# Kernel optimization log

Hardware: AMD Instinct MI355X
Metric: run time of the kernel (lower is better)

Reference implementation:

```python
import jax, jax.numpy as jnp
import numpy as np

B, MAX_H, MAX_W, D, S, HID = 64, 64, 32, 512, 8, 64


def setup_inputs() -> dict:
    key = jax.random.key(0)
    ks = jax.random.split(key, 7)
    return {
        "canonical": jax.random.normal(ks[0], (S, S, D), jnp.float32) * 0.02,
        "w1": jax.random.normal(ks[1], (2, HID), jnp.float32) * 0.5,
        "b1": jax.random.normal(ks[2], (HID,), jnp.float32) * 0.1,
        "w2": jax.random.normal(ks[3], (HID, D), jnp.float32) * 0.05,
        "b2": jax.random.normal(ks[4], (D,), jnp.float32) * 0.05,
        "batch_size": B,
        "target_h_list": jax.random.randint(ks[5], (B,), 1, MAX_H + 1, jnp.int32),
        "target_w_list": jax.random.randint(ks[6], (B,), 1, MAX_W + 1, jnp.int32),
        "max_h": MAX_H,
        "max_w": MAX_W,
    }


def _axis_coords(sizes, max_len):
    # sizes: [B] clamped lengths; returns normalized coords u in [0,1] at each
    # padded position (torch.linspace(0,1,L) semantics; 0 when L==1). [B, max_len]
    idx = jnp.arange(max_len, dtype=jnp.float32)[None, :]
    L = sizes[:, None].astype(jnp.float32)
    return jnp.where(L > 1, idx / jnp.maximum(L - 1.0, 1.0), 0.0)


def _forward(canonical, w1, b1, w2, b2, target_h_list, target_w_list, max_h, max_w):
    S_ = canonical.shape[0]
    Hs = jnp.clip(target_h_list, 1, max_h)  # [B]
    Ws = jnp.clip(target_w_list, 1, max_w)  # [B]

    u = _axis_coords(Hs, max_h)  # [B, mh]
    v = _axis_coords(Ws, max_w)  # [B, mw]

    # Bilinear resize of canonical grid with align_corners=True:
    # source coord = normalized coord * (S-1)
    sy = jnp.clip(u * (S_ - 1), 0.0, S_ - 1.0)  # [B, mh]
    sx = jnp.clip(v * (S_ - 1), 0.0, S_ - 1.0)  # [B, mw]
    y0 = jnp.floor(sy).astype(jnp.int32)
    x0 = jnp.floor(sx).astype(jnp.int32)
    y1 = jnp.minimum(y0 + 1, S_ - 1)
    x1 = jnp.minimum(x0 + 1, S_ - 1)
    wy = (sy - y0.astype(jnp.float32))[:, :, None, None]  # [B, mh, 1, 1]
    wx = (sx - x0.astype(jnp.float32))[:, None, :, None]  # [B, 1, mw, 1]

    yi0 = y0[:, :, None]  # [B, mh, 1]
    yi1 = y1[:, :, None]
    xi0 = x0[:, None, :]  # [B, 1, mw]
    xi1 = x1[:, None, :]
    q00 = canonical[yi0, xi0]  # [B, mh, mw, D]
    q01 = canonical[yi0, xi1]
    q10 = canonical[yi1, xi0]
    q11 = canonical[yi1, xi1]
    bil = ((1.0 - wy) * ((1.0 - wx) * q00 + wx * q01)
           + wy * ((1.0 - wx) * q10 + wx * q11))  # [B, mh, mw, D]

    # Coordinate refinement MLP on (u, v)
    coords = jnp.stack(
        [jnp.broadcast_to(u[:, :, None], (u.shape[0], max_h, max_w)),
         jnp.broadcast_to(v[:, None, :], (u.shape[0], max_h, max_w))],
        axis=-1)  # [B, mh, mw, 2]
    h = jax.nn.gelu(coords @ w1 + b1, approximate=False)
    delta = h @ w2 + b2  # [B, mh, mw, D]

    mask = ((jnp.arange(max_h)[None, :, None] < Hs[:, None, None])
            & (jnp.arange(max_w)[None, None, :] < Ws[:, None, None]))  # [B, mh, mw]
    queries = jnp.where(mask[..., None], bil + delta, 0.0)
    return queries, mask


def reference(canonical, w1, b1, w2, b2, batch_size, target_h_list,
              target_w_list, max_h, max_w):
    return _forward(canonical, w1, b1, w2, b2, target_h_list, target_w_list,
                    max_h, max_w)
```

## Files before the change

kernel.cpp:

```cpp
#include <hip/hip_runtime.h>
#include <math.h>

#define NB    64
#define MAXH  64
#define MAXW  32
#define DCH   512
#define SS    8
#define HID   64

#define QTOTAL ((size_t)NB * MAXH * MAXW * DCH)

typedef float f4 __attribute__((ext_vector_type(4)));

__device__ __forceinline__ float gelu_exact(float x) {
    return 0.5f * x * (1.0f + erff(x * 0.70710678118654752440f));
}

__global__ __launch_bounds__(256) void hgqg_kernel(
    const float* __restrict__ canonical,
    const float* __restrict__ w1,
    const float* __restrict__ b1,
    const float* __restrict__ w2,
    const float* __restrict__ b2,
    const int*   __restrict__ hlist,
    const int*   __restrict__ wlist,
    float* __restrict__ out)
{
    const int blk = blockIdx.x;
    const int b   = blk >> 6;
    const int i   = blk & 63;
    const int t   = threadIdx.x;

    int H = hlist[b]; H = min(max(H, 1), MAXH);
    int W = wlist[b]; W = min(max(W, 1), MAXW);

    f4* q4 = (f4*)(out + (size_t)blk * (MAXW * DCH));

    if (t < MAXW) {
        out[QTOTAL + (size_t)blk * MAXW + t] = (i < H && t < W) ? 1.0f : 0.0f;
    }

    if (i >= H) {
        const f4 z = {0.f, 0.f, 0.f, 0.f};
        #pragma unroll
        for (int r = 0; r < 16; ++r)
            __builtin_nontemporal_store(z, q4 + t + r * 256);
        return;
    }

    const float u    = (H > 1) ? (float)i / (float)(H - 1) : 0.0f;
    const float sy   = fminf(u * 7.0f, 7.0f);
    const int   y0   = (int)sy;
    const int   y1   = min(y0 + 1, SS - 1);
    const float wy   = sy - (float)y0;
    const float winv = (W > 1) ? 1.0f / (float)(W - 1) : 0.0f;

    __shared__ f4 ri[SS * 128];
    {
        const f4* can4 = (const f4*)canonical;
        #pragma unroll
        for (int r = 0; r < 4; ++r) {
            const int idx = t + r * 256;
            const int x   = idx >> 7;
            const int c   = idx & 127;
            const f4 a = can4[(y0 * SS + x) * 128 + c];
            const f4 d = can4[(y1 * SS + x) * 128 + c];
            ri[idx] = a + wy * (d - a);
        }
    }

    __shared__ __align__(16) float hsh[MAXW][HID];
    {
        const int j  = t >> 3;
        const int k0 = (t & 7) * 8;
        const float v = (float)j * winv;
        #pragma unroll
        for (int kk = 0; kk < 8; ++kk) {
            const int k = k0 + kk;
            hsh[j][k] = gelu_exact(u * w1[k] + v * w1[HID + k] + b1[k]);
        }
    }
    __syncthreads();

    const int cid = t & 127;
    const int jg  = t >> 7;
    const f4  bb2 = ((const f4*)b2)[cid];

    f4 acc[16];

    #pragma unroll
    for (int s = 0; s < 16; ++s) {
        const int   j  = jg + 2 * s;
        const float v  = (float)j * winv;
        const float sx = fminf(v * 7.0f, 7.0f);
        const int   x0 = (int)sx;
        const int   x1 = min(x0 + 1, SS - 1);
        const float wx = sx - (float)x0;
        const f4 f0 = ri[x0 * 128 + cid];
        const f4 f1 = ri[x1 * 128 + cid];
        acc[s] = f0 + wx * (f1 - f0) + bb2;
    }

    const f4* wp = (const f4*)w2 + cid;
    f4 wa = wp[0 * 128], wb = wp[1 * 128], wc = wp[2 * 128], wd = wp[3 * 128];
    #pragma unroll 1
    for (int kb = 0; kb < HID; kb += 4) {
        const int kn = (kb + 4 < HID) ? (kb + 4) : kb;
        const f4 na = wp[(kn + 0) * 128];
        const f4 nb = wp[(kn + 1) * 128];
        const f4 nc = wp[(kn + 2) * 128];
        const f4 nd = wp[(kn + 3) * 128];
        #pragma unroll
        for (int s = 0; s < 16; ++s) {
            const int j = jg + 2 * s;
            const f4 h4 = *(const f4*)&hsh[j][kb];
            acc[s] += h4.x * wa + h4.y * wb + h4.z * wc + h4.w * wd;
        }
        wa = na; wb = nb; wc = nc; wd = nd;
    }

    const f4 z = {0.f, 0.f, 0.f, 0.f};
    #pragma unroll
    for (int s = 0; s < 16; ++s) {
        const int j = jg + 2 * s;
        const f4 o = (j < W) ? acc[s] : z;
        __builtin_nontemporal_store(o, q4 + j * 128 + cid);
    }
}

extern "C" void kernel_launch(void* const* d_in, const int* in_sizes, int n_in,
                              void* d_out, int out_size, void* d_ws, size_t ws_size,
                              hipStream_t stream) {
    const float* canonical = (const float*)d_in[0];
    const float* w1        = (const float*)d_in[1];
    const float* b1        = (const float*)d_in[2];
    const float* w2        = (const float*)d_in[3];
    const float* b2        = (const float*)d_in[4];
    const int*   hlist     = (const int*)d_in[6];
    const int*   wlist     = (const int*)d_in[7];
    float* out = (float*)d_out;

    hgqg_kernel<<<NB * MAXH, 256, 0, stream>>>(
        canonical, w1, b1, w2, b2, hlist, wlist, out);
}
```

Baseline: 338.8 us.

## Precompute GELU hidden activations in a separate kernel and read them via scalar loads

```diff
diff --git a/kernel.cpp b/kernel.cpp
--- a/kernel.cpp
+++ b/kernel.cpp
@@ -16,14 +16,49 @@
     return 0.5f * x * (1.0f + erff(x * 0.70710678118654752440f));
 }
 
+__global__ __launch_bounds__(256) void hprep_kernel(
+    const float* __restrict__ w1,
+    const float* __restrict__ b1,
+    const int*   __restrict__ hlist,
+    const int*   __restrict__ wlist,
+    float* __restrict__ hg)
+{
+    const int T   = blockIdx.x * 256 + threadIdx.x;
+    const int s   = T & 15;
+    const int kq  = (T >> 4) & 15;
+    const int jg  = (T >> 8) & 1;
+    const int blk = T >> 9;
+    const int b   = blk >> 6;
+    const int i   = blk & 63;
+
+    int H = hlist[b]; H = min(max(H, 1), MAXH);
+    int W = wlist[b]; W = min(max(W, 1), MAXW);
+
+    const float u    = (H > 1) ? (float)i / (float)(H - 1) : 0.0f;
+    const float winv = (W > 1) ? 1.0f / (float)(W - 1) : 0.0f;
+    const int   j    = jg + 2 * s;
+    const float v    = (float)j * winv;
+
+    const f4 w1a = ((const f4*)w1)[kq];
+    const f4 w1b = ((const f4*)(w1 + HID))[kq];
+    const f4 b1v = ((const f4*)b1)[kq];
+
+    const f4 x = u * w1a + v * w1b + b1v;
+    f4 h;
+    h.x = gelu_exact(x.x);
+    h.y = gelu_exact(x.y);
+    h.z = gelu_exact(x.z);
+    h.w = gelu_exact(x.w);
+    ((f4*)hg)[T] = h;
+}
+
 __global__ __launch_bounds__(256) void hgqg_kernel(
     const float* __restrict__ canonical,
-    const float* __restrict__ w1,
-    const float* __restrict__ b1,
     const float* __restrict__ w2,
     const float* __restrict__ b2,
     const int*   __restrict__ hlist,
     const int*   __restrict__ wlist,
+    const float* __restrict__ hg,
     float* __restrict__ out)
 {
     const int blk = blockIdx.x;
@@ -40,11 +75,11 @@
         out[QTOTAL + (size_t)blk * MAXW + t] = (i < H && t < W) ? 1.0f : 0.0f;
     }
 
+    const f4 z = {0.f, 0.f, 0.f, 0.f};
+
     if (i >= H) {
-        const f4 z = {0.f, 0.f, 0.f, 0.f};
         #pragma unroll
-        for (int r = 0; r < 16; ++r)
-            __builtin_nontemporal_store(z, q4 + t + r * 256);
+        for (int r = 0; r < 16; ++r) q4[t + r * 256] = z;
         return;
     }
 
@@ -68,22 +103,10 @@
             ri[idx] = a + wy * (d - a);
         }
     }
-
-    __shared__ __align__(16) float hsh[MAXW][HID];
-    {
-        const int j  = t >> 3;
-        const int k0 = (t & 7) * 8;
-        const float v = (float)j * winv;
-        #pragma unroll
-        for (int kk = 0; kk < 8; ++kk) {
-            const int k = k0 + kk;
-            hsh[j][k] = gelu_exact(u * w1[k] + v * w1[HID + k] + b1[k]);
-        }
-    }
     __syncthreads();
 
     const int cid = t & 127;
-    const int jg  = t >> 7;
+    const int jg  = __builtin_amdgcn_readfirstlane(t >> 7);
     const f4  bb2 = ((const f4*)b2)[cid];
 
     f4 acc[16];
@@ -101,30 +124,30 @@
         acc[s] = f0 + wx * (f1 - f0) + bb2;
     }
 
-    const f4* wp = (const f4*)w2 + cid;
+    const f4* hb0 = (const f4*)hg + (((size_t)blk * 2 + jg) << 8);
+    const f4* wp  = (const f4*)w2 + cid;
+
     f4 wa = wp[0 * 128], wb = wp[1 * 128], wc = wp[2 * 128], wd = wp[3 * 128];
     #pragma unroll 1
-    for (int kb = 0; kb < HID; kb += 4) {
-        const int kn = (kb + 4 < HID) ? (kb + 4) : kb;
+    for (int kq = 0; kq < 16; ++kq) {
+        const int kn = (kq < 15) ? (4 * kq + 4) : (4 * kq);
         const f4 na = wp[(kn + 0) * 128];
         const f4 nb = wp[(kn + 1) * 128];
         const f4 nc = wp[(kn + 2) * 128];
         const f4 nd = wp[(kn + 3) * 128];
+        const f4* hb = hb0 + (kq << 4);
         #pragma unroll
         for (int s = 0; s < 16; ++s) {
-            const int j = jg + 2 * s;
-            const f4 h4 = *(const f4*)&hsh[j][kb];
+            const f4 h4 = hb[s];
             acc[s] += h4.x * wa + h4.y * wb + h4.z * wc + h4.w * wd;
         }
         wa = na; wb = nb; wc = nc; wd = nd;
     }
 
-    const f4 z = {0.f, 0.f, 0.f, 0.f};
     #pragma unroll
     for (int s = 0; s < 16; ++s) {
         const int j = jg + 2 * s;
-        const f4 o = (j < W) ? acc[s] : z;
-        __builtin_nontemporal_store(o, q4 + j * 128 + cid);
+        q4[j * 128 + cid] = (j < W) ? acc[s] : z;
     }
 }
 
@@ -139,7 +162,9 @@
     const int*   hlist     = (const int*)d_in[6];
     const int*   wlist     = (const int*)d_in[7];
     float* out = (float*)d_out;
+    float* hg  = (float*)d_ws;
 
+    hprep_kernel<<<8192, 256, 0, stream>>>(w1, b1, hlist, wlist, hg);
     hgqg_kernel<<<NB * MAXH, 256, 0, stream>>>(
-        canonical, w1, b1, w2, b2, hlist, wlist, out);
+        canonical, w2, b2, hlist, wlist, hg, out);
 }
```

After: 376.0 us. +11.0%, slower.

## Split each row block into two column halves and skip masked column work

Applied to the files above, without the earlier changes.

```diff
diff --git a/kernel.cpp b/kernel.cpp
--- a/kernel.cpp
+++ b/kernel.cpp
@@ -26,25 +26,30 @@
     const int*   __restrict__ wlist,
     float* __restrict__ out)
 {
-    const int blk = blockIdx.x;
-    const int b   = blk >> 6;
-    const int i   = blk & 63;
-    const int t   = threadIdx.x;
+    const int raw  = blockIdx.x;
+    const int id   = (raw ^ (raw >> 7)) & 8191;
+    const int i    = id & 63;
+    const int half = (id >> 6) & 1;
+    const int b    = id >> 7;
+    const int blk  = (b << 6) | i;
+    const int t    = threadIdx.x;
 
     int H = hlist[b]; H = min(max(H, 1), MAXH);
     int W = wlist[b]; W = min(max(W, 1), MAXW);
 
-    f4* q4 = (f4*)(out + (size_t)blk * (MAXW * DCH));
+    const int jbase = half << 4;
 
-    if (t < MAXW) {
+    f4* q4 = (f4*)(out + (size_t)blk * (MAXW * DCH)) + jbase * 128;
+
+    if (half == 0 && t < MAXW) {
         out[QTOTAL + (size_t)blk * MAXW + t] = (i < H && t < W) ? 1.0f : 0.0f;
     }
 
-    if (i >= H) {
-        const f4 z = {0.f, 0.f, 0.f, 0.f};
+    const f4 z = {0.f, 0.f, 0.f, 0.f};
+
+    if (i >= H || jbase >= W) {
         #pragma unroll
-        for (int r = 0; r < 16; ++r)
-            __builtin_nontemporal_store(z, q4 + t + r * 256);
+        for (int r = 0; r < 8; ++r) q4[t + r * 256] = z;
         return;
     }
 
@@ -55,29 +60,15 @@
     const float wy   = sy - (float)y0;
     const float winv = (W > 1) ? 1.0f / (float)(W - 1) : 0.0f;
 
-    __shared__ f4 ri[SS * 128];
+    __shared__ __align__(16) float hsh[16][HID];
     {
-        const f4* can4 = (const f4*)canonical;
+        const int jl = t >> 4;
+        const int k0 = (t & 15) * 4;
+        const float v = (float)(jbase + jl) * winv;
         #pragma unroll
-        for (int r = 0; r < 4; ++r) {
-            const int idx = t + r * 256;
-            const int x   = idx >> 7;
-            const int c   = idx & 127;
-            const f4 a = can4[(y0 * SS + x) * 128 + c];
-            const f4 d = can4[(y1 * SS + x) * 128 + c];
-            ri[idx] = a + wy * (d - a);
-        }
-    }
-
-    __shared__ __align__(16) float hsh[MAXW][HID];
-    {
-        const int j  = t >> 3;
-        const int k0 = (t & 7) * 8;
-        const float v = (float)j * winv;
-        #pragma unroll
-        for (int kk = 0; kk < 8; ++kk) {
+        for (int kk = 0; kk < 4; ++kk) {
             const int k = k0 + kk;
-            hsh[j][k] = gelu_exact(u * w1[k] + v * w1[HID + k] + b1[k]);
+            hsh[jl][k] = gelu_exact(u * w1[k] + v * w1[HID + k] + b1[k]);
         }
     }
     __syncthreads();
@@ -85,46 +76,54 @@
     const int cid = t & 127;
     const int jg  = t >> 7;
     const f4  bb2 = ((const f4*)b2)[cid];
+    const f4* can4 = (const f4*)canonical;
+    const f4* wp   = (const f4*)w2 + cid;
 
-    f4 acc[16];
+    f4 acc[8];
+    #pragma unroll
+    for (int s = 0; s < 8; ++s) acc[s] = z;
+
+    if (jbase + jg < W) {
+        #pragma unroll
+        for (int s = 0; s < 8; ++s) {
+            const int j = jbase + jg + 2 * s;
+            if (j < W) {
+                const float v  = (float)j * winv;
+                const float sx = fminf(v * 7.0f, 7.0f);
+                const int   x0 = (int)sx;
+                const int   x1 = min(x0 + 1, SS - 1);
+                const float wx = sx - (float)x0;
+                const f4 q00 = can4[(y0 * SS + x0) * 128 + cid];
+                const f4 q01 = can4[(y0 * SS + x1) * 128 + cid];
+                const f4 q10 = can4[(y1 * SS + x0) * 128 + cid];
+                const f4 q11 = can4[(y1 * SS + x1) * 128 + cid];
+                const f4 t0 = q00 + wx * (q01 - q00);
+                const f4 t1 = q10 + wx * (q11 - q10);
+                acc[s] = t0 + wy * (t1 - t0) + bb2;
+            }
+        }
+        #pragma unroll 1
+        for (int kb = 0; kb < HID; kb += 4) {
+            const f4 wa = wp[(kb + 0) * 128];
+            const f4 wb = wp[(kb + 1) * 128];
+            const f4 wc = wp[(kb + 2) * 128];
+            const f4 wd = wp[(kb + 3) * 128];
+            #pragma unroll
+            for (int s = 0; s < 8; ++s) {
+                const int j = jbase + jg + 2 * s;
+                if (j < W) {
+                    const int jl = jg + 2 * s;
+                    const f4 h4 = *(const f4*)&hsh[jl][kb];
+                    acc[s] += h4.x * wa + h4.y * wb + h4.z * wc + h4.w * wd;
+                }
+            }
+        }
+    }
 
     #pragma unroll
-    for (int s = 0; s < 16; ++s) {
-        const int   j  = jg + 2 * s;
-        const float v  = (float)j * winv;
-        const float sx = fminf(v * 7.0f, 7.0f);
-        const int   x0 = (int)sx;
-        const int   x1 = min(x0 + 1, SS - 1);
-        const float wx = sx - (float)x0;
-        const f4 f0 = ri[x0 * 128 + cid];
-        const f4 f1 = ri[x1 * 128 + cid];
-        acc[s] = f0 + wx * (f1 - f0) + bb2;
-    }
-
-    const f4* wp = (const f4*)w2 + cid;
-    f4 wa = wp[0 * 128], wb = wp[1 * 128], wc = wp[2 * 128], wd = wp[3 * 128];
-    #pragma unroll 1
-    for (int kb = 0; kb < HID; kb += 4) {
-        const int kn = (kb + 4 < HID) ? (kb + 4) : kb;
-        const f4 na = wp[(kn + 0) * 128];
-        const f4 nb = wp[(kn + 1) * 128];
-        const f4 nc = wp[(kn + 2) * 128];
-        const f4 nd = wp[(kn + 3) * 128];
-        #pragma unroll
-        for (int s = 0; s < 16; ++s) {
-            const int j = jg + 2 * s;
-            const f4 h4 = *(const f4*)&hsh[j][kb];
-            acc[s] += h4.x * wa + h4.y * wb + h4.z * wc + h4.w * wd;
-        }
-        wa = na; wb = nb; wc = nc; wd = nd;
-    }
-
-    const f4 z = {0.f, 0.f, 0.f, 0.f};
-    #pragma unroll
-    for (int s = 0; s < 16; ++s) {
+    for (int s = 0; s < 8; ++s) {
         const int j = jg + 2 * s;
-        const f4 o = (j < W) ? acc[s] : z;
-        __builtin_nontemporal_store(o, q4 + j * 128 + cid);
+        q4[j * 128 + cid] = acc[s];
     }
 }
 
@@ -140,6 +139,6 @@
     const int*   wlist     = (const int*)d_in[7];
     float* out = (float*)d_out;
 
-    hgqg_kernel<<<NB * MAXH, 256, 0, stream>>>(
+    hgqg_kernel<<<2 * NB * MAXH, 256, 0, stream>>>(
         canonical, w1, b1, w2, b2, hlist, wlist, out);
 }
```

Result: faster. 306.9 us (-9.4%).
